# Kernel optimization log

Measured on AMD Instinct MI355X. Metric: run time of the kernel, lower is better.

## Reference

```python
import jax, jax.numpy as jnp
import numpy as np

B, T, E, H = 8, 2048, 128, 4
FACTOR = 3  # autocorr_factor


def setup_inputs() -> dict:
    key = jax.random.key(0)
    ks = jax.random.split(key, 9)
    s = 0.05
    return {
        "hidden_states": jax.random.normal(ks[0], (B, T, E), jnp.float32),
        "wq": jax.random.normal(ks[1], (E, E, H), jnp.float32) * s,
        "bq": jax.random.normal(ks[2], (E, H), jnp.float32) * s,
        "wk": jax.random.normal(ks[3], (E, E, H), jnp.float32) * s,
        "bk": jax.random.normal(ks[4], (E, H), jnp.float32) * s,
        "wv": jax.random.normal(ks[5], (E, E, H), jnp.float32) * s,
        "bv": jax.random.normal(ks[6], (E, H), jnp.float32) * s,
        "wo": jax.random.normal(ks[7], (E, H, E), jnp.float32) * s,
        "bo": jax.random.normal(ks[8], (E,), jnp.float32) * s,
    }


def reference(hidden_states, wq, bq, wk, bk, wv, bv, wo, bo):
    # Inference path (training=None) of AutoCorrelation.call
    bsize, seq_len, _ = hidden_states.shape
    q = jnp.einsum('btj,juh->btuh', hidden_states, wq) + bq  # [B,T,E,H]
    k = jnp.einsum('btj,juh->btuh', hidden_states, wk) + bk
    v = jnp.einsum('btj,juh->btuh', hidden_states, wv) + bv

    # FFT cross-correlation over time axis
    qf = jnp.fft.rfft(q.transpose(0, 2, 3, 1), n=seq_len, axis=-1)  # [B,E,H,F]
    kf = jnp.fft.rfft(k.transpose(0, 2, 3, 1), n=seq_len, axis=-1)
    ac = jnp.fft.irfft(qf * jnp.conj(kf), n=seq_len, axis=-1)       # [B,E,H,T]
    ac = ac.transpose(0, 3, 1, 2)                                   # [B,T,E,H]

    ac_mean = ac.mean(axis=-1)                                      # [B,T,E]
    top_k = int(FACTOR * np.log(float(seq_len)))

    # top-k delays per (batch, channel)
    vals, idx = jax.lax.top_k(ac_mean.transpose(0, 2, 1), top_k)    # [B,E,K]
    w = jax.nn.softmax(vals, axis=-1)  # == Softmax(axis=-2) on [B,K,E]

    # NOTE: in the source, `delays_agg +=` is dedented outside the top_k loop,
    # so only the LAST iteration (i = top_k-1) contributes. Replicated faithfully.
    delay = idx[:, :, top_k - 1]   # [B,E] int
    wgt = w[:, :, top_k - 1]       # [B,E]

    # gather over doubled values == circular roll by -delay per (b, channel)
    t_idx = (jnp.arange(seq_len)[None, :, None] + delay[:, None, :]) % seq_len  # [B,T,E]
    rolled = jnp.take_along_axis(v, t_idx[..., None], axis=1)       # [B,T,E,H]
    agg = rolled * wgt[:, None, :, None]                            # [B,T,E,H]

    return jnp.einsum('btjh,jhf->btf', agg, wo) + bo                # [B,T,E]
```

## Files before the change

kernel.cpp:

```cpp
#include <hip/hip_runtime.h>
#include <math.h>

#define TSEQ 2048
#define BB 8
#define EE 128
#define HH 4
#define UHN 512
#define KTOP 22
#define BT (BB*TSEQ)
#define APITCH 40
#define OPITCH 76

typedef _Float16 f16;
typedef f16 f16x2 __attribute__((ext_vector_type(2)));
typedef f16 f16x4 __attribute__((ext_vector_type(4)));
typedef f16 f16x8 __attribute__((ext_vector_type(8)));
typedef float f32x4 __attribute__((ext_vector_type(4)));

__device__ __forceinline__ float2 cmul(float2 a, float2 b) {
  return make_float2(a.x*b.x - a.y*b.y, a.x*b.y + a.y*b.x);
}
__device__ __forceinline__ float2 cadd(float2 a, float2 b) {
  return make_float2(a.x + b.x, a.y + b.y);
}
__device__ __forceinline__ float2 csub(float2 a, float2 b) {
  return make_float2(a.x - b.x, a.y - b.y);
}

__device__ __forceinline__ f16x8 ld_frag(const f16* p) {
  f16x4 lo = *(const f16x4*)(p);
  f16x4 hi = *(const f16x4*)(p + 16);
  return __builtin_shufflevector(lo, hi, 0, 1, 2, 3, 4, 5, 6, 7);
}

__global__ __launch_bounds__(256)
void prep_kernel(const float* __restrict__ hs,
                 const float* __restrict__ wq, const float* __restrict__ wk,
                 const float* __restrict__ wv, const float* __restrict__ wo,
                 f16* __restrict__ hs_h, f16* __restrict__ hs_l,
                 f16* __restrict__ Wt_h, f16* __restrict__ Wt_l,
                 f16* __restrict__ wo_t)
{
  __shared__ float tile[64][65];
  const int bx = blockIdx.x, tid = threadIdx.x;

  if (bx < 1024) {
    size_t base = ((size_t)bx*256 + tid) * 8;
    float4 a = *(const float4*)&hs[base];
    float4 b = *(const float4*)&hs[base + 4];
    float vf[8] = {a.x,a.y,a.z,a.w, b.x,b.y,b.z,b.w};
    f16 h[8], l[8];
#pragma unroll
    for (int j = 0; j < 8; ++j) { h[j] = (f16)vf[j]; l[j] = (f16)(vf[j] - (float)h[j]); }
    *(f16x8*)&hs_h[base] = (f16x8){h[0],h[1],h[2],h[3],h[4],h[5],h[6],h[7]};
    *(f16x8*)&hs_l[base] = (f16x8){l[0],l[1],l[2],l[3],l[4],l[5],l[6],l[7]};
  } else if (bx < 1072) {
    int r = bx - 1024;
    int z = r >> 4, rem = r & 15, kt = rem & 1, uht = rem >> 1;
    const float* W = (z == 0) ? wq : (z == 1) ? wk : wv;
#pragma unroll
    for (int rr = 0; rr < 16; ++rr) {
      int idx = tid + 256*rr;
      int krow = idx >> 6, ucol = idx & 63;
      tile[krow][ucol] = W[(size_t)(kt*64 + krow)*UHN + uht*64 + ucol];
    }
    __syncthreads();
#pragma unroll
    for (int rr = 0; rr < 16; ++rr) {
      int idx = tid + 256*rr;
      int orow = idx >> 6, ocol = idx & 63;
      float w = tile[ocol][orow];
      f16 h = (f16)w;
      size_t o = ((size_t)z*UHN + uht*64 + orow)*EE + kt*64 + ocol;
      Wt_h[o] = h;
      Wt_l[o] = (f16)(w - (float)h);
    }
  } else {
    int r = bx - 1072;
    int ft = r & 1, uht = r >> 1;
#pragma unroll
    for (int rr = 0; rr < 16; ++rr) {
      int idx = tid + 256*rr;
      int urow = idx >> 6, fcol = idx & 63;
      tile[urow][fcol] = wo[(size_t)(uht*64 + urow)*EE + ft*64 + fcol];
    }
    __syncthreads();
#pragma unroll
    for (int rr = 0; rr < 16; ++rr) {
      int idx = tid + 256*rr;
      int orow = idx >> 6, ocol = idx & 63;
      wo_t[(size_t)(ft*64 + orow)*UHN + uht*64 + ocol] = (f16)tile[ocol][orow];
    }
  }
}

__global__ __launch_bounds__(256, 3)
void proj_mfma(const f16* __restrict__ hs_h, const f16* __restrict__ hs_l,
               const f16* __restrict__ Wt_h, const f16* __restrict__ Wt_l,
               const float* __restrict__ bq, const float* __restrict__ bk,
               const float* __restrict__ bv,
               float* __restrict__ q_t, float* __restrict__ k_t, f16* __restrict__ v_t)
{
  __shared__ f16 Ah[128*APITCH];
  __shared__ f16 Al[128*APITCH];
  __shared__ f16 Bh[128*APITCH];
  __shared__ f16 Bl[128*APITCH];

  const int z = blockIdx.z;
  const float* bias = (z == 0) ? bq : (z == 1) ? bk : bv;
  const f16* WH = Wt_h + (size_t)z*UHN*EE;
  const f16* WL = Wt_l + (size_t)z*UHN*EE;

  const int tid  = threadIdx.x;
  const int lane = tid & 63, wid = tid >> 6;
  const int wm = wid >> 1, wn = wid & 1;
  const int ln15 = lane & 15, g = lane >> 4;
  const int uh0 = blockIdx.x * 128;
  const int bt0 = blockIdx.y * 128;

  f32x4 acc[4][4] = {};

  for (int kc = 0; kc < 4; ++kc) {
    const int k0 = kc * 32;
    __syncthreads();
#pragma unroll
    for (int r = 0; r < 2; ++r) {
      int idx = tid + 256*r;
      int row = idx >> 2, seg = (idx & 3) << 3;
      size_t ga = (size_t)(uh0 + row)*EE + k0 + seg;
      *(f16x8*)&Ah[row*APITCH + seg] = *(const f16x8*)&WH[ga];
      *(f16x8*)&Al[row*APITCH + seg] = *(const f16x8*)&WL[ga];
      size_t gb = (size_t)(bt0 + row)*EE + k0 + seg;
      *(f16x8*)&Bh[row*APITCH + seg] = *(const f16x8*)&hs_h[gb];
      *(f16x8*)&Bl[row*APITCH + seg] = *(const f16x8*)&hs_l[gb];
    }
    __syncthreads();
    const int kb = 4*g;
    f16x8 a_h[4], a_l[4], b_h[4], b_l[4];
#pragma unroll
    for (int mf = 0; mf < 4; ++mf) {
      int off = (wm*64 + mf*16 + ln15)*APITCH + kb;
      a_h[mf] = ld_frag(&Ah[off]);
      a_l[mf] = ld_frag(&Al[off]);
    }
#pragma unroll
    for (int nf = 0; nf < 4; ++nf) {
      int off = (wn*64 + nf*16 + ln15)*APITCH + kb;
      b_h[nf] = ld_frag(&Bh[off]);
      b_l[nf] = ld_frag(&Bl[off]);
    }
#pragma unroll
    for (int mf = 0; mf < 4; ++mf)
#pragma unroll
      for (int nf = 0; nf < 4; ++nf) {
        acc[mf][nf] = __builtin_amdgcn_mfma_f32_16x16x32_f16(a_h[mf], b_h[nf], acc[mf][nf], 0, 0, 0);
        acc[mf][nf] = __builtin_amdgcn_mfma_f32_16x16x32_f16(a_h[mf], b_l[nf], acc[mf][nf], 0, 0, 0);
        acc[mf][nf] = __builtin_amdgcn_mfma_f32_16x16x32_f16(a_l[mf], b_h[nf], acc[mf][nf], 0, 0, 0);
      }
  }

  const int b = bt0 >> 11, tb = bt0 & (TSEQ - 1);
  if (z == 2) {
#pragma unroll
    for (int mf = 0; mf < 4; ++mf) {
      int uhb = uh0 + wm*64 + mf*16 + g*4;
      f32x4 bias4 = *(const f32x4*)&bias[uhb];
#pragma unroll
      for (int r = 0; r < 4; ++r) {
        f16* vrow = v_t + ((size_t)(b*UHN + uhb + r))*TSEQ + tb;
#pragma unroll
        for (int nf = 0; nf < 4; ++nf)
          vrow[wn*64 + nf*16 + ln15] = (f16)(acc[mf][nf][r] + bias4[r]);
      }
    }
  } else {
    float* outp = (z == 0) ? q_t : k_t;
#pragma unroll
    for (int mf = 0; mf < 4; ++mf) {
      int uhb = uh0 + wm*64 + mf*16 + g*4;
      f32x4 bias4 = *(const f32x4*)&bias[uhb];
#pragma unroll
      for (int r = 0; r < 4; ++r) {
        size_t rowbase = ((size_t)(b*UHN + uhb + r))*TSEQ + tb;
#pragma unroll
        for (int nf = 0; nf < 4; ++nf)
          outp[rowbase + wn*64 + nf*16 + ln15] = acc[mf][nf][r] + bias4[r];
      }
    }
  }
}

#define ZPAD(g) ((g) + ((g) >> 5))

template<int SGN>
__device__ __forceinline__ float2 addim(float2 a, float2 b) {
  return (SGN < 0) ? make_float2(a.x + b.y, a.y - b.x)
                   : make_float2(a.x - b.y, a.y + b.x);
}
template<int SGN>
__device__ __forceinline__ float2 subim(float2 a, float2 b) {
  return (SGN < 0) ? make_float2(a.x - b.y, a.y + b.x)
                   : make_float2(a.x + b.y, a.y - b.x);
}

template<int SGN>
__device__ __forceinline__ void dft8(const float2* u, float2* y) {
  const float r2 = 0.70710678118654752440f;
  float2 a0 = cadd(u[0], u[4]), a1 = cadd(u[1], u[5]);
  float2 a2 = cadd(u[2], u[6]), a3 = cadd(u[3], u[7]);
  float2 b0 = csub(u[0], u[4]), b1 = csub(u[1], u[5]);
  float2 b2 = csub(u[2], u[6]), b3 = csub(u[3], u[7]);
  float2 t1 = (SGN < 0) ? make_float2(r2*(b1.x + b1.y), r2*(b1.y - b1.x))
                        : make_float2(r2*(b1.x - b1.y), r2*(b1.y + b1.x));
  float2 t2 = (SGN < 0) ? make_float2(b2.y, -b2.x) : make_float2(-b2.y, b2.x);
  float2 e  = (SGN < 0) ? make_float2(r2*(b3.x + b3.y), r2*(b3.y - b3.x))
                        : make_float2(r2*(b3.x - b3.y), r2*(b3.y + b3.x));
  float2 t3 = (SGN < 0) ? make_float2(e.y, -e.x) : make_float2(-e.y, e.x);
  {
    float2 c0 = cadd(a0, a2), c1 = csub(a0, a2);
    float2 c2 = cadd(a1, a3), c3 = csub(a1, a3);
    y[0] = cadd(c0, c2); y[4] = csub(c0, c2);
    y[2] = addim<SGN>(c1, c3); y[6] = subim<SGN>(c1, c3);
  }
  {
    float2 c0 = cadd(b0, t2), c1 = csub(b0, t2);
    float2 c2 = cadd(t1, t3), c3 = csub(t1, t3);
    y[1] = cadd(c0, c2); y[5] = csub(c0, c2);
    y[3] = addim<SGN>(c1, c3); y[7] = subim<SGN>(c1, c3);
  }
}

__device__ __forceinline__ void fwd_radix8(float2* Z, float2 w1, int base, int eighth) {
  float2 u[8];
#pragma unroll
  for (int t = 0; t < 8; ++t) u[t] = Z[ZPAD(base + eighth*t)];
  float2 y[8];
  dft8<-1>(u, y);
  Z[ZPAD(base)] = y[0];
  float2 w = w1;
  Z[ZPAD(base + eighth)] = cmul(y[1], w);
#pragma unroll
  for (int s = 2; s < 8; ++s) {
    w = cmul(w, w1);
    Z[ZPAD(base + eighth*s)] = cmul(y[s], w);
  }
}

__device__ __forceinline__ void inv_radix8(float2* Z, float2 w1c, int base, int eighth) {
  float2 u[8];
#pragma unroll
  for (int t = 0; t < 8; ++t) u[t] = Z[ZPAD(base + eighth*t)];
  u[1] = cmul(u[1], w1c);
  float2 w = w1c;
#pragma unroll
  for (int t = 2; t < 8; ++t) {
    w = cmul(w, w1c);
    u[t] = cmul(u[t], w);
  }
  float2 y[8];
  dft8<1>(u, y);
#pragma unroll
  for (int s = 0; s < 8; ++s) Z[ZPAD(base + eighth*s)] = y[s];
}

template<int SGN>
__device__ __forceinline__ void radix4_stage(float2* Z, int base) {
  float2 v0 = Z[ZPAD(base)], v1 = Z[ZPAD(base+1)];
  float2 v2 = Z[ZPAD(base+2)], v3 = Z[ZPAD(base+3)];
  float2 c0 = cadd(v0, v2), c1 = csub(v0, v2);
  float2 c2 = cadd(v1, v3), c3 = csub(v1, v3);
  Z[ZPAD(base)]   = cadd(c0, c2);
  Z[ZPAD(base+1)] = addim<SGN>(c1, c3);
  Z[ZPAD(base+2)] = csub(c0, c2);
  Z[ZPAD(base+3)] = subim<SGN>(c1, c3);
}

__global__ __launch_bounds__(256)
void fftcorr_topk(const float* __restrict__ q_t, const float* __restrict__ k_t,
                  int* __restrict__ delay, float* __restrict__ wgt)
{
  __shared__ float2 Z[2112];
  __shared__ float2 twl[292];
  __shared__ float rv[4];
  __shared__ int   ri[4];

  const int tid = threadIdx.x;
  const int bu  = blockIdx.x;

  for (int idx = tid; idx < 292; idx += 256) {
    float ang;
    if (idx < 256)      ang = -6.2831853071795864769f * (float)idx / 2048.0f;
    else if (idx < 288) ang = -6.2831853071795864769f * (float)(idx - 256) / 256.0f;
    else                ang = -6.2831853071795864769f * (float)(idx - 288) / 32.0f;
    float s, c;
    sincosf(ang, &s, &c);
    twl[idx] = make_float2(c, s);
  }
  const float2* tw1 = twl;
  const float2* tw2 = twl + 256;
  const float2* tw3 = twl + 288;

  int pp[8];
#pragma unroll
  for (int r = 0; r < 8; ++r) {
    int p = tid + (r << 8);
    int f = ((p >> 8) & 7) | (((p >> 5) & 7) << 3) | (((p >> 2) & 7) << 6) | ((p & 3) << 9);
    int nf = (2048 - f) & 2047;
    pp[r] = ((nf & 7) << 8) | (((nf >> 3) & 7) << 5) | (((nf >> 6) & 7) << 2) | ((nf >> 9) & 3);
  }
  float2 sreg[8] = {};
  __syncthreads();

  for (int h = 0; h < HH; ++h) {
    const float* qp = q_t + ((size_t)bu*HH + h)*TSEQ;
    const float* kp = k_t + ((size_t)bu*HH + h)*TSEQ;
    {
      float2 u[8];
#pragma unroll
      for (int t = 0; t < 8; ++t)
        u[t] = make_float2(qp[tid + 256*t], kp[tid + 256*t]);
      float2 y[8];
      dft8<-1>(u, y);
      float2 w1 = tw1[tid];
      Z[ZPAD(tid)] = y[0];
      float2 w = w1;
      Z[ZPAD(tid + 256)] = cmul(y[1], w);
#pragma unroll
      for (int s = 2; s < 8; ++s) {
        w = cmul(w, w1);
        Z[ZPAD(tid + 256*s)] = cmul(y[s], w);
      }
    }
    __syncthreads();
    fwd_radix8(Z, tw2[tid & 31], ((tid >> 5) << 8) + (tid & 31), 32);
    __syncthreads();
    fwd_radix8(Z, tw3[tid & 3], ((tid >> 2) << 5) + (tid & 3), 4);
    __syncthreads();
    radix4_stage<-1>(Z, 4*tid);
    radix4_stage<-1>(Z, 4*(tid + 256));
    __syncthreads();
#pragma unroll
    for (int r = 0; r < 8; ++r) {
      int p = tid + (r << 8);
      float2 A  = Z[ZPAD(p)];
      float2 Zp = Z[ZPAD(pp[r])];
      sreg[r].x += 0.5f  * (Zp.x*A.y + Zp.y*A.x);
      sreg[r].y += 0.25f * ((A.x*A.x + A.y*A.y) - (Zp.x*Zp.x + Zp.y*Zp.y));
    }
    __syncthreads();
  }

#pragma unroll
  for (int r = 0; r < 8; ++r) Z[ZPAD(tid + (r << 8))] = sreg[r];
  __syncthreads();
  radix4_stage<1>(Z, 4*tid);
  radix4_stage<1>(Z, 4*(tid + 256));
  __syncthreads();
  { float2 w = tw3[tid & 3]; w.y = -w.y;
    inv_radix8(Z, w, ((tid >> 2) << 5) + (tid & 3), 4); }
  __syncthreads();
  { float2 w = tw2[tid & 31]; w.y = -w.y;
    inv_radix8(Z, w, ((tid >> 5) << 8) + (tid & 31), 32); }
  __syncthreads();

  float* vbuf = (float*)Z;
  {
    float2 u[8];
#pragma unroll
    for (int t = 0; t < 8; ++t) u[t] = Z[ZPAD(tid + 256*t)];
    __syncthreads();
    float2 w1c = tw1[tid]; w1c.y = -w1c.y;
    u[1] = cmul(u[1], w1c);
    float2 w = w1c;
#pragma unroll
    for (int t = 2; t < 8; ++t) {
      w = cmul(w, w1c);
      u[t] = cmul(u[t], w);
    }
    float2 y[8];
    dft8<1>(u, y);
    const float scale = 1.0f / (float)(TSEQ * HH);
#pragma unroll
    for (int s = 0; s < 8; ++s)
      vbuf[tid + 256*s] = y[s].x * scale;
  }

  float m0 = 0.f, ssum = 0.f;
  for (int it = 0; it < KTOP; ++it) {
    __syncthreads();
    float best = -3.4e38f; int bi = 0;
#pragma unroll
    for (int r = 0; r < 8; ++r) {
      int i = tid + 256*r;
      float x = vbuf[i];
      if (x > best) { best = x; bi = i; }
    }
#pragma unroll
    for (int off = 32; off > 0; off >>= 1) {
      float ob = __shfl_down(best, off);
      int   oi = __shfl_down(bi, off);
      if (ob > best || (ob == best && oi < bi)) { best = ob; bi = oi; }
    }
    if ((tid & 63) == 0) { rv[tid >> 6] = best; ri[tid >> 6] = bi; }
    __syncthreads();
    if (tid == 0) {
      float gb = rv[0]; int gi = ri[0];
      for (int w2 = 1; w2 < 4; ++w2)
        if (rv[w2] > gb || (rv[w2] == gb && ri[w2] < gi)) { gb = rv[w2]; gi = ri[w2]; }
      vbuf[gi] = -3.4e38f;
      if (it == 0) m0 = gb;
      ssum += expf(gb - m0);
      if (it == KTOP - 1) {
        delay[bu] = gi;
        wgt[bu]   = expf(gb - m0) / ssum;
      }
    }
  }
}

__global__ __launch_bounds__(256)
void out_mfma(const f16* __restrict__ v_t, const int* __restrict__ delay,
              const float* __restrict__ wgt, const f16* __restrict__ wo_t,
              const float* __restrict__ bo, float* __restrict__ out)
{
  __shared__ f16 Af[64*OPITCH];
  __shared__ f16 Bf[64*OPITCH];
  __shared__ int   dly[EE];
  __shared__ float wg[EE];

  const int tid  = threadIdx.x;
  const int lane = tid & 63, wid = tid >> 6;
  const int wm = wid >> 1, wn = wid & 1;
  const int ln15 = lane & 15, g = lane >> 4;
  const int t0g = blockIdx.x * 64;
  const int f0  = blockIdx.y * 64;
  const int b = t0g >> 11, t0 = t0g & (TSEQ - 1);

  if (tid < EE) { dly[tid] = delay[b*EE + tid]; wg[tid] = wgt[b*EE + tid]; }

  f32x4 acc[2][2] = {};

  for (int c = 0; c < 8; ++c) {
    const int uh0 = c * 64;
    __syncthreads();
#pragma unroll
    for (int r = 0; r < 16; ++r) {
      int idx = tid + 256*r;
      int tl = idx & 63, ul = idx >> 6;
      int u = (uh0 + ul) >> 2;
      float x = (float)v_t[((size_t)(b*UHN + uh0 + ul))*TSEQ + ((t0 + tl + dly[u]) & (TSEQ-1))]
                * wg[u];
      Af[tl*OPITCH + ul] = (f16)x;
    }
#pragma unroll
    for (int r = 0; r < 2; ++r) {
      int idx = tid + 256*r;
      int fl = idx >> 3, seg = (idx & 7) << 3;
      const f16* src = &wo_t[(size_t)(f0 + fl)*UHN + uh0 + seg];
      *(f16x4*)&Bf[fl*OPITCH + seg]     = *(const f16x4*)(src);
      *(f16x4*)&Bf[fl*OPITCH + seg + 4] = *(const f16x4*)(src + 4);
    }
    __syncthreads();
#pragma unroll
    for (int ks = 0; ks < 2; ++ks) {
      const int kb = ks*32 + 4*g;
      f16x8 av[2], bv[2];
#pragma unroll
      for (int mf = 0; mf < 2; ++mf)
        av[mf] = ld_frag(&Af[(wm*32 + mf*16 + ln15)*OPITCH + kb]);
#pragma unroll
      for (int nf = 0; nf < 2; ++nf)
        bv[nf] = ld_frag(&Bf[(wn*32 + nf*16 + ln15)*OPITCH + kb]);
#pragma unroll
      for (int mf = 0; mf < 2; ++mf)
#pragma unroll
        for (int nf = 0; nf < 2; ++nf)
          acc[mf][nf] = __builtin_amdgcn_mfma_f32_16x16x32_f16(av[mf], bv[nf], acc[mf][nf], 0, 0, 0);
    }
  }

#pragma unroll
  for (int mf = 0; mf < 2; ++mf)
#pragma unroll
    for (int r = 0; r < 4; ++r) {
      int bt = t0g + wm*32 + mf*16 + g*4 + r;
#pragma unroll
      for (int nf = 0; nf < 2; ++nf) {
        int f = f0 + wn*32 + nf*16 + ln15;
        out[(size_t)bt*EE + f] = acc[mf][nf][r] + bo[f];
      }
    }
}

extern "C" void kernel_launch(void* const* d_in, const int* in_sizes, int n_in,
                              void* d_out, int out_size, void* d_ws, size_t ws_size,
                              hipStream_t stream) {
  (void)in_sizes; (void)n_in; (void)out_size; (void)ws_size;
  const float* hs = (const float*)d_in[0];
  const float* wq = (const float*)d_in[1];
  const float* bq = (const float*)d_in[2];
  const float* wk = (const float*)d_in[3];
  const float* bk = (const float*)d_in[4];
  const float* wv = (const float*)d_in[5];
  const float* bv = (const float*)d_in[6];
  const float* wo = (const float*)d_in[7];
  const float* bo = (const float*)d_in[8];
  float* out = (float*)d_out;

  char* p = (char*)d_ws;
  float* q_t  = (float*)p;  p += (size_t)BB*UHN*TSEQ*4;
  float* k_t  = (float*)p;  p += (size_t)BB*UHN*TSEQ*4;
  f16*   v_t  = (f16*)p;    p += (size_t)BB*UHN*TSEQ*2;
  f16*   hs_h = (f16*)p;    p += (size_t)BT*EE*2;
  f16*   hs_l = (f16*)p;    p += (size_t)BT*EE*2;
  f16*   Wt_h = (f16*)p;    p += (size_t)3*UHN*EE*2;
  f16*   Wt_l = (f16*)p;    p += (size_t)3*UHN*EE*2;
  f16*   wo_t = (f16*)p;    p += (size_t)EE*UHN*2;
  int*   delay = (int*)p;   p += BB*EE*4;
  float* wgt   = (float*)p;

  prep_kernel<<<dim3(1088), 256, 0, stream>>>(hs, wq, wk, wv, wo,
                                              hs_h, hs_l, Wt_h, Wt_l, wo_t);
  proj_mfma<<<dim3(4, 128, 3), 256, 0, stream>>>(hs_h, hs_l, Wt_h, Wt_l,
                                                 bq, bk, bv, q_t, k_t, v_t);
  fftcorr_topk<<<dim3(1024), 256, 0, stream>>>(q_t, k_t, delay, wgt);
  out_mfma<<<dim3(256, 2), 256, 0, stream>>>(v_t, delay, wgt, wo_t, bo, out);
}
```

Measured before the change: 119.7 us.

## Pack two channels per FFT block and use single-wave incremental top-k selection

The FFT correlation kernel now handles two (batch, channel) rows per 512-thread block, each half working on its own region of shared memory. Top-k selection changes from 22 block-wide reductions, each with barriers, to a per-thread local max cached in shared memory. A single wavefront then reduces those maxima each round and rescans only the column that lost its maximum. The projection kernel's occupancy hint is also raised from 3 to 4, which may force register spills.

```diff
diff --git a/kernel.cpp b/kernel.cpp
--- a/kernel.cpp
+++ b/kernel.cpp
@@ -94,7 +94,7 @@
   }
 }
 
-__global__ __launch_bounds__(256, 3)
+__global__ __launch_bounds__(256, 4)
 void proj_mfma(const f16* __restrict__ hs_h, const f16* __restrict__ hs_l,
                const f16* __restrict__ Wt_h, const f16* __restrict__ Wt_l,
                const float* __restrict__ bq, const float* __restrict__ bk,
@@ -275,19 +275,21 @@
   Z[ZPAD(base+3)] = subim<SGN>(c1, c3);
 }
 
-__global__ __launch_bounds__(256)
+__global__ __launch_bounds__(512, 8)
 void fftcorr_topk(const float* __restrict__ q_t, const float* __restrict__ k_t,
                   int* __restrict__ delay, float* __restrict__ wgt)
 {
-  __shared__ float2 Z[2112];
+  __shared__ float2 Z[2*2112];
   __shared__ float2 twl[292];
-  __shared__ float rv[4];
-  __shared__ int   ri[4];
-
-  const int tid = threadIdx.x;
-  const int bu  = blockIdx.x;
-
-  for (int idx = tid; idx < 292; idx += 256) {
+
+  const int tid  = threadIdx.x;
+  const int half = tid >> 8;
+  const int t8   = tid & 255;
+  const int bu   = blockIdx.x*2 + half;
+  float2* Zh = Z + half*2112;
+
+  if (tid < 292) {
+    int idx = tid;
     float ang;
     if (idx < 256)      ang = -6.2831853071795864769f * (float)idx / 2048.0f;
     else if (idx < 288) ang = -6.2831853071795864769f * (float)(idx - 256) / 256.0f;
@@ -303,7 +305,7 @@
   int pp[8];
 #pragma unroll
   for (int r = 0; r < 8; ++r) {
-    int p = tid + (r << 8);
+    int p = t8 + (r << 8);
     int f = ((p >> 8) & 7) | (((p >> 5) & 7) << 3) | (((p >> 2) & 7) << 6) | ((p & 3) << 9);
     int nf = (2048 - f) & 2047;
     pp[r] = ((nf & 7) << 8) | (((nf >> 3) & 7) << 5) | (((nf >> 6) & 7) << 2) | ((nf >> 9) & 3);
@@ -318,32 +320,32 @@
       float2 u[8];
 #pragma unroll
       for (int t = 0; t < 8; ++t)
-        u[t] = make_float2(qp[tid + 256*t], kp[tid + 256*t]);
+        u[t] = make_float2(qp[t8 + 256*t], kp[t8 + 256*t]);
       float2 y[8];
       dft8<-1>(u, y);
-      float2 w1 = tw1[tid];
-      Z[ZPAD(tid)] = y[0];
+      float2 w1 = tw1[t8];
+      Zh[ZPAD(t8)] = y[0];
       float2 w = w1;
-      Z[ZPAD(tid + 256)] = cmul(y[1], w);
+      Zh[ZPAD(t8 + 256)] = cmul(y[1], w);
 #pragma unroll
       for (int s = 2; s < 8; ++s) {
         w = cmul(w, w1);
-        Z[ZPAD(tid + 256*s)] = cmul(y[s], w);
-      }
-    }
-    __syncthreads();
-    fwd_radix8(Z, tw2[tid & 31], ((tid >> 5) << 8) + (tid & 31), 32);
-    __syncthreads();
-    fwd_radix8(Z, tw3[tid & 3], ((tid >> 2) << 5) + (tid & 3), 4);
-    __syncthreads();
-    radix4_stage<-1>(Z, 4*tid);
-    radix4_stage<-1>(Z, 4*(tid + 256));
+        Zh[ZPAD(t8 + 256*s)] = cmul(y[s], w);
+      }
+    }
+    __syncthreads();
+    fwd_radix8(Zh, tw2[t8 & 31], ((t8 >> 5) << 8) + (t8 & 31), 32);
+    __syncthreads();
+    fwd_radix8(Zh, tw3[t8 & 3], ((t8 >> 2) << 5) + (t8 & 3), 4);
+    __syncthreads();
+    radix4_stage<-1>(Zh, 4*t8);
+    radix4_stage<-1>(Zh, 4*(t8 + 256));
     __syncthreads();
 #pragma unroll
     for (int r = 0; r < 8; ++r) {
-      int p = tid + (r << 8);
-      float2 A  = Z[ZPAD(p)];
-      float2 Zp = Z[ZPAD(pp[r])];
+      int p = t8 + (r << 8);
+      float2 A  = Zh[ZPAD(p)];
+      float2 Zp = Zh[ZPAD(pp[r])];
       sreg[r].x += 0.5f  * (Zp.x*A.y + Zp.y*A.x);
       sreg[r].y += 0.25f * ((A.x*A.x + A.y*A.y) - (Zp.x*Zp.x + Zp.y*Zp.y));
     }
@@ -351,25 +353,27 @@
   }
 
 #pragma unroll
-  for (int r = 0; r < 8; ++r) Z[ZPAD(tid + (r << 8))] = sreg[r];
+  for (int r = 0; r < 8; ++r) Zh[ZPAD(t8 + (r << 8))] = sreg[r];
   __syncthreads();
-  radix4_stage<1>(Z, 4*tid);
-  radix4_stage<1>(Z, 4*(tid + 256));
+  radix4_stage<1>(Zh, 4*t8);
+  radix4_stage<1>(Zh, 4*(t8 + 256));
   __syncthreads();
-  { float2 w = tw3[tid & 3]; w.y = -w.y;
-    inv_radix8(Z, w, ((tid >> 2) << 5) + (tid & 3), 4); }
+  { float2 w = tw3[t8 & 3]; w.y = -w.y;
+    inv_radix8(Zh, w, ((t8 >> 2) << 5) + (t8 & 3), 4); }
   __syncthreads();
-  { float2 w = tw2[tid & 31]; w.y = -w.y;
-    inv_radix8(Z, w, ((tid >> 5) << 8) + (tid & 31), 32); }
+  { float2 w = tw2[t8 & 31]; w.y = -w.y;
+    inv_radix8(Zh, w, ((t8 >> 5) << 8) + (t8 & 31), 32); }
   __syncthreads();
 
-  float* vbuf = (float*)Z;
+  float* vbuf = (float*)Zh;
+  float* lmf  = vbuf + 2048;
+  int*   lii  = (int*)(vbuf + 2304);
   {
     float2 u[8];
 #pragma unroll
-    for (int t = 0; t < 8; ++t) u[t] = Z[ZPAD(tid + 256*t)];
-    __syncthreads();
-    float2 w1c = tw1[tid]; w1c.y = -w1c.y;
+    for (int t = 0; t < 8; ++t) u[t] = Zh[ZPAD(t8 + 256*t)];
+    __syncthreads();
+    float2 w1c = tw1[t8]; w1c.y = -w1c.y;
     u[1] = cmul(u[1], w1c);
     float2 w = w1c;
 #pragma unroll
@@ -380,39 +384,56 @@
     float2 y[8];
     dft8<1>(u, y);
     const float scale = 1.0f / (float)(TSEQ * HH);
-#pragma unroll
-    for (int s = 0; s < 8; ++s)
-      vbuf[tid + 256*s] = y[s].x * scale;
-  }
-
-  float m0 = 0.f, ssum = 0.f;
-  for (int it = 0; it < KTOP; ++it) {
-    __syncthreads();
-    float best = -3.4e38f; int bi = 0;
-#pragma unroll
-    for (int r = 0; r < 8; ++r) {
-      int i = tid + 256*r;
-      float x = vbuf[i];
-      if (x > best) { best = x; bi = i; }
-    }
-#pragma unroll
-    for (int off = 32; off > 0; off >>= 1) {
-      float ob = __shfl_down(best, off);
-      int   oi = __shfl_down(bi, off);
-      if (ob > best || (ob == best && oi < bi)) { best = ob; bi = oi; }
-    }
-    if ((tid & 63) == 0) { rv[tid >> 6] = best; ri[tid >> 6] = bi; }
-    __syncthreads();
-    if (tid == 0) {
-      float gb = rv[0]; int gi = ri[0];
-      for (int w2 = 1; w2 < 4; ++w2)
-        if (rv[w2] > gb || (rv[w2] == gb && ri[w2] < gi)) { gb = rv[w2]; gi = ri[w2]; }
-      vbuf[gi] = -3.4e38f;
-      if (it == 0) m0 = gb;
-      ssum += expf(gb - m0);
-      if (it == KTOP - 1) {
-        delay[bu] = gi;
-        wgt[bu]   = expf(gb - m0) / ssum;
+    float lb = -3.4e38f; int lbi = t8;
+#pragma unroll
+    for (int s = 0; s < 8; ++s) {
+      float x = y[s].x * scale;
+      vbuf[t8 + 256*s] = x;
+      if (x > lb) { lb = x; lbi = t8 + 256*s; }
+    }
+    lmf[t8] = lb;
+    lii[t8] = lbi;
+  }
+  __syncthreads();
+
+  if (((tid >> 6) & 3) == 0) {
+    const int lane = tid & 63;
+    float m0 = 0.f, ssum = 0.f;
+    for (int it = 0; it < KTOP; ++it) {
+      float best = -3.4e38f; int bi = 0x40000000;
+#pragma unroll
+      for (int e = 0; e < 4; ++e) {
+        float x = lmf[4*lane + e];
+        int  xi = lii[4*lane + e];
+        if (x > best || (x == best && xi < bi)) { best = x; bi = xi; }
+      }
+#pragma unroll
+      for (int off = 32; off > 0; off >>= 1) {
+        float ob = __shfl_down(best, off);
+        int   oi = __shfl_down(bi, off);
+        if (ob > best || (ob == best && oi < bi)) { best = ob; bi = oi; }
+      }
+      float gb = __shfl(best, 0);
+      int   gi = __shfl(bi, 0);
+      int   ow = gi & 255;
+      if (lane == (ow >> 2)) {
+        vbuf[gi] = -3.4e38f;
+        float nb = -3.4e38f; int ni = ow;
+#pragma unroll
+        for (int s = 0; s < 8; ++s) {
+          float x = vbuf[ow + 256*s];
+          if (x > nb) { nb = x; ni = ow + 256*s; }
+        }
+        lmf[ow] = nb;
+        lii[ow] = ni;
+      }
+      if (lane == 0) {
+        if (it == 0) m0 = gb;
+        ssum += expf(gb - m0);
+        if (it == KTOP - 1) {
+          delay[bu] = gi;
+          wgt[bu]   = expf(gb - m0) / ssum;
+        }
       }
     }
   }
@@ -523,6 +544,6 @@
                                               hs_h, hs_l, Wt_h, Wt_l, wo_t);
   proj_mfma<<<dim3(4, 128, 3), 256, 0, stream>>>(hs_h, hs_l, Wt_h, Wt_l,
                                                  bq, bk, bv, q_t, k_t, v_t);
-  fftcorr_topk<<<dim3(1024), 256, 0, stream>>>(q_t, k_t, delay, wgt);
+  fftcorr_topk<<<dim3(512), 512, 0, stream>>>(q_t, k_t, delay, wgt);
   out_mfma<<<dim3(256, 2), 256, 0, stream>>>(v_t, delay, wgt, wo_t, bo, out);
 }
```

Measured after the change: 172.9 us. 44.4% more time.

## Rework top-k selection into single-wave incremental argmax and vectorize FFT math

Applied to the files above, without the earlier changes.

The 22-iteration top-k loop, which used two block-wide barriers per iteration, becomes a single-wavefront search. It works over per-thread cached maxima and rescans only the owning thread's 8 values after each removal. The FFT helpers switch to 2-wide vector types, twiddle powers are computed with a shallower tree instead of a serial chain, and one barrier per head iteration is dropped. The intent is to cut synchronization and serial latency in the FFT correlation kernel, at the cost of more LDS traffic in the single wave and a slightly different twiddle rounding order.

```diff
diff --git a/kernel.cpp b/kernel.cpp
--- a/kernel.cpp
+++ b/kernel.cpp
@@ -16,15 +16,16 @@
 typedef f16 f16x4 __attribute__((ext_vector_type(4)));
 typedef f16 f16x8 __attribute__((ext_vector_type(8)));
 typedef float f32x4 __attribute__((ext_vector_type(4)));
-
-__device__ __forceinline__ float2 cmul(float2 a, float2 b) {
-  return make_float2(a.x*b.x - a.y*b.y, a.x*b.y + a.y*b.x);
-}
-__device__ __forceinline__ float2 cadd(float2 a, float2 b) {
-  return make_float2(a.x + b.x, a.y + b.y);
-}
-__device__ __forceinline__ float2 csub(float2 a, float2 b) {
-  return make_float2(a.x - b.x, a.y - b.y);
+typedef float cpx  __attribute__((ext_vector_type(2)));
+
+__device__ __forceinline__ cpx cmul(cpx a, cpx b) {
+  cpx r = (cpx){a.x, a.x} * b;
+  r += (cpx){-a.y, a.y} * (cpx){b.y, b.x};
+  return r;
+}
+template<int SGN>
+__device__ __forceinline__ cpx muli(cpx b) {
+  return (SGN < 0) ? (cpx){b.y, -b.x} : (cpx){-b.y, b.x};
 }
 
 __device__ __forceinline__ f16x8 ld_frag(const f16* p) {
@@ -193,96 +194,88 @@
 #define ZPAD(g) ((g) + ((g) >> 5))
 
 template<int SGN>
-__device__ __forceinline__ float2 addim(float2 a, float2 b) {
-  return (SGN < 0) ? make_float2(a.x + b.y, a.y - b.x)
-                   : make_float2(a.x - b.y, a.y + b.x);
-}
+__device__ __forceinline__ void dft8(const cpx* u, cpx* y) {
+  const float r2 = 0.70710678118654752440f;
+  cpx a0 = u[0] + u[4], a1 = u[1] + u[5];
+  cpx a2 = u[2] + u[6], a3 = u[3] + u[7];
+  cpx b0 = u[0] - u[4], b1 = u[1] - u[5];
+  cpx b2 = u[2] - u[6], b3 = u[3] - u[7];
+  cpx t1 = (b1 + muli<SGN>(b1)) * r2;
+  cpx t2 = muli<SGN>(b2);
+  cpx e  = (b3 + muli<SGN>(b3)) * r2;
+  cpx t3 = muli<SGN>(e);
+  {
+    cpx c0 = a0 + a2, c1 = a0 - a2;
+    cpx c2 = a1 + a3, c3 = a1 - a3;
+    y[0] = c0 + c2; y[4] = c0 - c2;
+    y[2] = c1 + muli<SGN>(c3); y[6] = c1 - muli<SGN>(c3);
+  }
+  {
+    cpx c0 = b0 + t2, c1 = b0 - t2;
+    cpx c2 = t1 + t3, c3 = t1 - t3;
+    y[1] = c0 + c2; y[5] = c0 - c2;
+    y[3] = c1 + muli<SGN>(c3); y[7] = c1 - muli<SGN>(c3);
+  }
+}
+
+__device__ __forceinline__ void wpow_tree(cpx w1, cpx* W) {
+  W[0] = w1;
+  cpx w2 = cmul(w1, w1);
+  cpx w4 = cmul(w2, w2);
+  W[1] = w2;
+  W[2] = cmul(w2, w1);
+  W[3] = w4;
+  W[4] = cmul(w4, w1);
+  W[5] = cmul(w4, w2);
+  W[6] = cmul(w4, W[2]);
+}
+
+__device__ __forceinline__ void fwd_radix8(cpx* Z, cpx w1, int base, int eighth) {
+  cpx u[8];
+#pragma unroll
+  for (int t = 0; t < 8; ++t) u[t] = Z[ZPAD(base + eighth*t)];
+  cpx y[8];
+  dft8<-1>(u, y);
+  cpx W[7];
+  wpow_tree(w1, W);
+  Z[ZPAD(base)] = y[0];
+#pragma unroll
+  for (int s = 1; s < 8; ++s)
+    Z[ZPAD(base + eighth*s)] = cmul(y[s], W[s-1]);
+}
+
+__device__ __forceinline__ void inv_radix8(cpx* Z, cpx w1c, int base, int eighth) {
+  cpx u[8];
+#pragma unroll
+  for (int t = 0; t < 8; ++t) u[t] = Z[ZPAD(base + eighth*t)];
+  cpx W[7];
+  wpow_tree(w1c, W);
+#pragma unroll
+  for (int t = 1; t < 8; ++t) u[t] = cmul(u[t], W[t-1]);
+  cpx y[8];
+  dft8<1>(u, y);
+#pragma unroll
+  for (int s = 0; s < 8; ++s) Z[ZPAD(base + eighth*s)] = y[s];
+}
+
 template<int SGN>
-__device__ __forceinline__ float2 subim(float2 a, float2 b) {
-  return (SGN < 0) ? make_float2(a.x - b.y, a.y + b.x)
-                   : make_float2(a.x + b.y, a.y - b.x);
-}
-
-template<int SGN>
-__device__ __forceinline__ void dft8(const float2* u, float2* y) {
-  const float r2 = 0.70710678118654752440f;
-  float2 a0 = cadd(u[0], u[4]), a1 = cadd(u[1], u[5]);
-  float2 a2 = cadd(u[2], u[6]), a3 = cadd(u[3], u[7]);
-  float2 b0 = csub(u[0], u[4]), b1 = csub(u[1], u[5]);
-  float2 b2 = csub(u[2], u[6]), b3 = csub(u[3], u[7]);
-  float2 t1 = (SGN < 0) ? make_float2(r2*(b1.x + b1.y), r2*(b1.y - b1.x))
-                        : make_float2(r2*(b1.x - b1.y), r2*(b1.y + b1.x));
-  float2 t2 = (SGN < 0) ? make_float2(b2.y, -b2.x) : make_float2(-b2.y, b2.x);
-  float2 e  = (SGN < 0) ? make_float2(r2*(b3.x + b3.y), r2*(b3.y - b3.x))
-                        : make_float2(r2*(b3.x - b3.y), r2*(b3.y + b3.x));
-  float2 t3 = (SGN < 0) ? make_float2(e.y, -e.x) : make_float2(-e.y, e.x);
-  {
-    float2 c0 = cadd(a0, a2), c1 = csub(a0, a2);
-    float2 c2 = cadd(a1, a3), c3 = csub(a1, a3);
-    y[0] = cadd(c0, c2); y[4] = csub(c0, c2);
-    y[2] = addim<SGN>(c1, c3); y[6] = subim<SGN>(c1, c3);
-  }
-  {
-    float2 c0 = cadd(b0, t2), c1 = csub(b0, t2);
-    float2 c2 = cadd(t1, t3), c3 = csub(t1, t3);
-    y[1] = cadd(c0, c2); y[5] = csub(c0, c2);
-    y[3] = addim<SGN>(c1, c3); y[7] = subim<SGN>(c1, c3);
-  }
-}
-
-__device__ __forceinline__ void fwd_radix8(float2* Z, float2 w1, int base, int eighth) {
-  float2 u[8];
-#pragma unroll
-  for (int t = 0; t < 8; ++t) u[t] = Z[ZPAD(base + eighth*t)];
-  float2 y[8];
-  dft8<-1>(u, y);
-  Z[ZPAD(base)] = y[0];
-  float2 w = w1;
-  Z[ZPAD(base + eighth)] = cmul(y[1], w);
-#pragma unroll
-  for (int s = 2; s < 8; ++s) {
-    w = cmul(w, w1);
-    Z[ZPAD(base + eighth*s)] = cmul(y[s], w);
-  }
-}
-
-__device__ __forceinline__ void inv_radix8(float2* Z, float2 w1c, int base, int eighth) {
-  float2 u[8];
-#pragma unroll
-  for (int t = 0; t < 8; ++t) u[t] = Z[ZPAD(base + eighth*t)];
-  u[1] = cmul(u[1], w1c);
-  float2 w = w1c;
-#pragma unroll
-  for (int t = 2; t < 8; ++t) {
-    w = cmul(w, w1c);
-    u[t] = cmul(u[t], w);
-  }
-  float2 y[8];
-  dft8<1>(u, y);
-#pragma unroll
-  for (int s = 0; s < 8; ++s) Z[ZPAD(base + eighth*s)] = y[s];
-}
-
-template<int SGN>
-__device__ __forceinline__ void radix4_stage(float2* Z, int base) {
-  float2 v0 = Z[ZPAD(base)], v1 = Z[ZPAD(base+1)];
-  float2 v2 = Z[ZPAD(base+2)], v3 = Z[ZPAD(base+3)];
-  float2 c0 = cadd(v0, v2), c1 = csub(v0, v2);
-  float2 c2 = cadd(v1, v3), c3 = csub(v1, v3);
-  Z[ZPAD(base)]   = cadd(c0, c2);
-  Z[ZPAD(base+1)] = addim<SGN>(c1, c3);
-  Z[ZPAD(base+2)] = csub(c0, c2);
-  Z[ZPAD(base+3)] = subim<SGN>(c1, c3);
+__device__ __forceinline__ void radix4_stage(cpx* Z, int base) {
+  cpx v0 = Z[ZPAD(base)], v1 = Z[ZPAD(base+1)];
+  cpx v2 = Z[ZPAD(base+2)], v3 = Z[ZPAD(base+3)];
+  cpx c0 = v0 + v2, c1 = v0 - v2;
+  cpx c2 = v1 + v3, c3 = v1 - v3;
+  Z[ZPAD(base)]   = c0 + c2;
+  Z[ZPAD(base+1)] = c1 + muli<SGN>(c3);
+  Z[ZPAD(base+2)] = c0 - c2;
+  Z[ZPAD(base+3)] = c1 - muli<SGN>(c3);
 }
 
 __global__ __launch_bounds__(256)
 void fftcorr_topk(const float* __restrict__ q_t, const float* __restrict__ k_t,
                   int* __restrict__ delay, float* __restrict__ wgt)
 {
-  __shared__ float2 Z[2112];
-  __shared__ float2 twl[292];
-  __shared__ float rv[4];
-  __shared__ int   ri[4];
+  __shared__ cpx Z[2112];
+  __shared__ cpx twl[292];
 
   const int tid = threadIdx.x;
   const int bu  = blockIdx.x;
@@ -294,11 +287,11 @@
     else                ang = -6.2831853071795864769f * (float)(idx - 288) / 32.0f;
     float s, c;
     sincosf(ang, &s, &c);
-    twl[idx] = make_float2(c, s);
-  }
-  const float2* tw1 = twl;
-  const float2* tw2 = twl + 256;
-  const float2* tw3 = twl + 288;
+    twl[idx] = (cpx){c, s};
+  }
+  const cpx* tw1 = twl;
+  const cpx* tw2 = twl + 256;
+  const cpx* tw3 = twl + 288;
 
   int pp[8];
 #pragma unroll
@@ -308,28 +301,26 @@
     int nf = (2048 - f) & 2047;
     pp[r] = ((nf & 7) << 8) | (((nf >> 3) & 7) << 5) | (((nf >> 6) & 7) << 2) | ((nf >> 9) & 3);
   }
-  float2 sreg[8] = {};
+  cpx sreg[8] = {};
   __syncthreads();
 
   for (int h = 0; h < HH; ++h) {
     const float* qp = q_t + ((size_t)bu*HH + h)*TSEQ;
     const float* kp = k_t + ((size_t)bu*HH + h)*TSEQ;
+    if (h) __syncthreads();
     {
-      float2 u[8];
+      cpx u[8];
 #pragma unroll
       for (int t = 0; t < 8; ++t)
-        u[t] = make_float2(qp[tid + 256*t], kp[tid + 256*t]);
-      float2 y[8];
+        u[t] = (cpx){qp[tid + 256*t], kp[tid + 256*t]};
+      cpx y[8];
       dft8<-1>(u, y);
-      float2 w1 = tw1[tid];
+      cpx W[7];
+      wpow_tree(tw1[tid], W);
       Z[ZPAD(tid)] = y[0];
-      float2 w = w1;
-      Z[ZPAD(tid + 256)] = cmul(y[1], w);
-#pragma unroll
-      for (int s = 2; s < 8; ++s) {
-        w = cmul(w, w1);
-        Z[ZPAD(tid + 256*s)] = cmul(y[s], w);
-      }
+#pragma unroll
+      for (int s = 1; s < 8; ++s)
+        Z[ZPAD(tid + 256*s)] = cmul(y[s], W[s-1]);
     }
     __syncthreads();
     fwd_radix8(Z, tw2[tid & 31], ((tid >> 5) << 8) + (tid & 31), 32);
@@ -342,13 +333,13 @@
 #pragma unroll
     for (int r = 0; r < 8; ++r) {
       int p = tid + (r << 8);
-      float2 A  = Z[ZPAD(p)];
-      float2 Zp = Z[ZPAD(pp[r])];
+      cpx A  = Z[ZPAD(p)];
+      cpx Zp = Z[ZPAD(pp[r])];
       sreg[r].x += 0.5f  * (Zp.x*A.y + Zp.y*A.x);
       sreg[r].y += 0.25f * ((A.x*A.x + A.y*A.y) - (Zp.x*Zp.x + Zp.y*Zp.y));
     }
-    __syncthreads();
-  }
+  }
+  __syncthreads();
 
 #pragma unroll
   for (int r = 0; r < 8; ++r) Z[ZPAD(tid + (r << 8))] = sreg[r];
@@ -356,63 +347,79 @@
   radix4_stage<1>(Z, 4*tid);
   radix4_stage<1>(Z, 4*(tid + 256));
   __syncthreads();
-  { float2 w = tw3[tid & 3]; w.y = -w.y;
+  { cpx w = tw3[tid & 3]; w.y = -w.y;
     inv_radix8(Z, w, ((tid >> 2) << 5) + (tid & 3), 4); }
   __syncthreads();
-  { float2 w = tw2[tid & 31]; w.y = -w.y;
+  { cpx w = tw2[tid & 31]; w.y = -w.y;
     inv_radix8(Z, w, ((tid >> 5) << 8) + (tid & 31), 32); }
   __syncthreads();
 
   float* vbuf = (float*)Z;
+  float* lmf  = vbuf + 2048;
+  int*   lii  = (int*)(vbuf + 2304);
   {
-    float2 u[8];
+    cpx u[8];
 #pragma unroll
     for (int t = 0; t < 8; ++t) u[t] = Z[ZPAD(tid + 256*t)];
     __syncthreads();
-    float2 w1c = tw1[tid]; w1c.y = -w1c.y;
-    u[1] = cmul(u[1], w1c);
-    float2 w = w1c;
-#pragma unroll
-    for (int t = 2; t < 8; ++t) {
-      w = cmul(w, w1c);
-      u[t] = cmul(u[t], w);
-    }
-    float2 y[8];
+    cpx w1c = tw1[tid]; w1c.y = -w1c.y;
+    cpx W[7];
+    wpow_tree(w1c, W);
+#pragma unroll
+    for (int t = 1; t < 8; ++t) u[t] = cmul(u[t], W[t-1]);
+    cpx y[8];
     dft8<1>(u, y);
     const float scale = 1.0f / (float)(TSEQ * HH);
-#pragma unroll
-    for (int s = 0; s < 8; ++s)
-      vbuf[tid + 256*s] = y[s].x * scale;
-  }
-
-  float m0 = 0.f, ssum = 0.f;
-  for (int it = 0; it < KTOP; ++it) {
-    __syncthreads();
-    float best = -3.4e38f; int bi = 0;
-#pragma unroll
-    for (int r = 0; r < 8; ++r) {
-      int i = tid + 256*r;
-      float x = vbuf[i];
-      if (x > best) { best = x; bi = i; }
-    }
-#pragma unroll
-    for (int off = 32; off > 0; off >>= 1) {
-      float ob = __shfl_down(best, off);
-      int   oi = __shfl_down(bi, off);
-      if (ob > best || (ob == best && oi < bi)) { best = ob; bi = oi; }
-    }
-    if ((tid & 63) == 0) { rv[tid >> 6] = best; ri[tid >> 6] = bi; }
-    __syncthreads();
-    if (tid == 0) {
-      float gb = rv[0]; int gi = ri[0];
-      for (int w2 = 1; w2 < 4; ++w2)
-        if (rv[w2] > gb || (rv[w2] == gb && ri[w2] < gi)) { gb = rv[w2]; gi = ri[w2]; }
-      vbuf[gi] = -3.4e38f;
-      if (it == 0) m0 = gb;
-      ssum += expf(gb - m0);
-      if (it == KTOP - 1) {
-        delay[bu] = gi;
-        wgt[bu]   = expf(gb - m0) / ssum;
+    float lb = -3.4e38f; int lbi = tid;
+#pragma unroll
+    for (int s = 0; s < 8; ++s) {
+      float x = y[s].x * scale;
+      vbuf[tid + 256*s] = x;
+      if (x > lb) { lb = x; lbi = tid + 256*s; }
+    }
+    lmf[tid] = lb;
+    lii[tid] = lbi;
+  }
+  __syncthreads();
+
+  if (tid < 64) {
+    const int lane = tid;
+    float m0 = 0.f, ssum = 0.f;
+    for (int it = 0; it < KTOP; ++it) {
+      float best = -3.4e38f; int bi = 0x40000000;
+#pragma unroll
+      for (int e = 0; e < 4; ++e) {
+        float x = lmf[4*lane + e];
+        int  xi = lii[4*lane + e];
+        if (x > best || (x == best && xi < bi)) { best = x; bi = xi; }
+      }
+#pragma unroll
+      for (int off = 32; off > 0; off >>= 1) {
+        float ob = __shfl_down(best, off);
+        int   oi = __shfl_down(bi, off);
+        if (ob > best || (ob == best && oi < bi)) { best = ob; bi = oi; }
+      }
+      float gb = __shfl(best, 0);
+      int   gi = __shfl(bi, 0);
+      int   ow = gi & 255;
+      if (lane == (ow >> 2)) {
+        vbuf[gi] = -3.4e38f;
+        float nb = -3.4e38f; int ni = ow;
+#pragma unroll
+        for (int s = 0; s < 8; ++s) {
+          float x = vbuf[ow + 256*s];
+          if (x > nb) { nb = x; ni = ow + 256*s; }
+        }
+        lmf[ow] = nb;
+        lii[ow] = ni;
+      }
+      if (lane == 0) {
+        if (it == 0) m0 = gb;
+        ssum += expf(gb - m0);
+        if (it == KTOP - 1) {
+          delay[bu] = gi;
+          wgt[bu]   = expf(gb - m0) / ssum;
+        }
       }
     }
   }
```

Result: faster. 116.1 us (median of 2 runs) (-3.1%).
